# Optimization experiments

Measured on AMD Instinct MI355X. Metric: run time of the kernel, lower is better.

## Reference

```python
import jax, jax.numpy as jnp
import numpy as np

N = 50000   # nodes
E = 800000  # edges
F = 128     # n_features
H = 128     # n_hidden
LN_EPS = 1e-5


def setup_inputs() -> dict:
    key = jax.random.key(0)
    ks = jax.random.split(key, 11)
    s = 0.05
    return {
        "x": jax.random.normal(ks[0], (N, F), jnp.float32),
        "edge_index": jax.random.randint(ks[1], (2, E), 0, N, dtype=jnp.int64),
        "edge_attr": jax.random.uniform(ks[2], (E, 1), jnp.float32),
        "ln_gamma": jax.random.normal(ks[3], (F,), jnp.float32),
        "ln_beta": jax.random.normal(ks[4], (F,), jnp.float32),
        "W1": jax.random.normal(ks[5], (F, H), jnp.float32) * s,
        "b1": jax.random.normal(ks[6], (H,), jnp.float32) * s,
        "W2": jax.random.normal(ks[7], (H, H), jnp.float32) * s,
        "b2": jax.random.normal(ks[8], (H,), jnp.float32) * s,
        "W3": jax.random.normal(ks[9], (H, 1), jnp.float32) * s,
        "b3": jax.random.normal(ks[10], (1,), jnp.float32) * s,
    }


def _gcn_conv(x, W, b, row, col, ew, n_nodes):
    """PyG GCNConv: add self loops (weight 1), symmetric normalization,
    gather-scale-scatter aggregation, linear (no bias) + bias."""
    loop = jnp.arange(n_nodes, dtype=row.dtype)
    row_f = jnp.concatenate([row, loop])          # [E+N] source
    col_f = jnp.concatenate([col, loop])          # [E+N] target
    ew_f = jnp.concatenate([ew, jnp.ones((n_nodes,), ew.dtype)])
    deg = jax.ops.segment_sum(ew_f, col_f, num_segments=n_nodes)  # [N]
    dis = jnp.where(deg > 0, jax.lax.rsqrt(jnp.where(deg > 0, deg, 1.0)), 0.0)
    norm = dis[row_f] * ew_f * dis[col_f]          # [E+N]
    h = x @ W                                      # [N, out]
    msg = h[row_f] * norm[:, None]                 # [E+N, out] gather+scale
    out = jax.ops.segment_sum(msg, col_f, num_segments=n_nodes)  # scatter-add
    return out + b


def reference(x, edge_index, edge_attr, ln_gamma, ln_beta, W1, b1, W2, b2, W3, b3):
    x = jnp.nan_to_num(x, nan=0.0, posinf=0.0, neginf=0.0)
    ew = jnp.nan_to_num(edge_attr[:, 0], nan=0.0, posinf=1.0, neginf=0.0)  # [E]
    row, col = edge_index[0], edge_index[1]
    # input LayerNorm
    mu = jnp.mean(x, axis=-1, keepdims=True)
    var = jnp.mean(jnp.square(x - mu), axis=-1, keepdims=True)
    x = (x - mu) * jax.lax.rsqrt(var + LN_EPS) * ln_gamma + ln_beta
    # hidden GCN layers (dropout = identity in eval mode)
    x = jax.nn.relu(_gcn_conv(x, W1, b1, row, col, ew, N))
    x = jax.nn.relu(_gcn_conv(x, W2, b2, row, col, ew, N))
    # output layer
    return _gcn_conv(x, W3, b3, row, col, ew, N)  # [N, 1]
```

## Files before the change

### kernel.cpp

```cpp
#include <hip/hip_runtime.h>
#include <hip/hip_fp16.h>
#include <math.h>

#define NNODES 50000
#define NEDGES 800000
#define NF 128
#define BK 128
constexpr float LN_EPS = 1e-5f;

typedef short v8s __attribute__((ext_vector_type(8)));
typedef unsigned short v8u __attribute__((ext_vector_type(8)));
typedef float v4f __attribute__((ext_vector_type(4)));

__device__ __forceinline__ float clean0(float v) {
    return (isnan(v) || isinf(v)) ? 0.0f : v;
}
__device__ __forceinline__ float cleanw(float v) {
    if (isnan(v)) return 0.0f;
    if (isinf(v)) return v > 0.0f ? 1.0f : 0.0f;
    return v;
}
__device__ __forceinline__ int clampN(int v) {
    return min(max(v, 0), NNODES - 1);
}
__device__ __forceinline__ int pad8(int v) { return (v + 7) & ~7; }

__device__ __forceinline__ unsigned short f2bf(float f) {
    unsigned int u = __float_as_uint(f);
    return (unsigned short)((u + 0x7FFFu + ((u >> 16) & 1u)) >> 16);
}
__device__ __forceinline__ float bf2f(unsigned short h) {
    return __uint_as_float(((unsigned int)h) << 16);
}
__device__ __forceinline__ void split_bf(float v, unsigned short& h, unsigned short& l) {
    h = f2bf(v);
    l = f2bf(v - bf2f(h));
}

__global__ void k_build_ln(const int* __restrict__ ei, const float* __restrict__ ea,
                           int* __restrict__ cnt4, int2* __restrict__ bucket,
                           const float* __restrict__ x, const float* __restrict__ gamma,
                           const float* __restrict__ beta, unsigned short* __restrict__ z,
                           int nbb) {
    if ((int)blockIdx.x < nbb) {
        int e = blockIdx.x * 256 + threadIdx.x;
        if (e >= NEDGES) return;
        int r = clampN(ei[e]);
        int c = clampN(ei[NEDGES + e]);
        float w = cleanw(ea[e]);
        int s = e & 3;
        int pos = atomicAdd(&cnt4[(c << 2) + s], 1);
        if (pos < 32) bucket[(c << 7) + (s << 5) + pos] = make_int2(r, __float_as_int(w));
    } else {
        int bid = blockIdx.x - nbb;
        int n = (bid * 256 + threadIdx.x) >> 6;
        int lane = threadIdx.x & 63;
        if (n >= NNODES) return;
        float2 v = ((const float2*)(x + (size_t)n * NF))[lane];
        v.x = clean0(v.x); v.y = clean0(v.y);
        float s = v.x + v.y;
        for (int o = 32; o > 0; o >>= 1) s += __shfl_xor(s, o);
        float mu = s * (1.0f / NF);
        float dx = v.x - mu, dy = v.y - mu;
        float q = dx * dx + dy * dy;
        for (int o = 32; o > 0; o >>= 1) q += __shfl_xor(q, o);
        float rstd = rsqrtf(q * (1.0f / NF) + LN_EPS);
        float2 g = ((const float2*)gamma)[lane];
        float2 b = ((const float2*)beta)[lane];
        float ox = dx * rstd * g.x + b.x;
        float oy = dy * rstd * g.y + b.y;
        ((__half2*)z)[(size_t)n * 64 + lane] = __float22half2_rn(make_float2(ox, oy));
    }
}

__global__ void k_prep(int2* __restrict__ bucket, const int* __restrict__ cnt4,
                       int* __restrict__ cntp, float* __restrict__ dis,
                       const float* __restrict__ W1, const float* __restrict__ W2,
                       unsigned short* __restrict__ Wh1T, unsigned short* __restrict__ Wl1T,
                       unsigned short* __restrict__ Wh2T, unsigned short* __restrict__ Wl2T,
                       int nbn) {
    if ((int)blockIdx.x < nbn) {
        int n = blockIdx.x * 256 + threadIdx.x;
        if (n >= NNODES) return;
        int4 c4 = ((const int4*)cnt4)[n];
        int cs[4] = { min(c4.x, 32), min(c4.y, 32), min(c4.z, 32), min(c4.w, 32) };
        int base = n << 7;
        float d = 1.0f;
        for (int i = 0; i < cs[0]; i++) d += __int_as_float(bucket[base + i].y);
        int total = cs[0];
        #pragma unroll
        for (int s = 1; s < 4; s++) {
            int src = base + (s << 5);
            for (int i = 0; i < cs[s]; i++) {
                int2 rec = bucket[src + i];
                d += __int_as_float(rec.y);
                bucket[base + total + i] = rec;
            }
            total += cs[s];
        }
        for (int p = total; p < pad8(total); p++) bucket[base + p] = make_int2(0, 0);
        dis[n] = rsqrtf(d);
        cntp[n] = pad8(total);
    } else {
        int idx = (blockIdx.x - nbn) * 256 + threadIdx.x;
        int m = idx >> 14;
        int n = (idx >> 7) & 127;
        int k = idx & 127;
        const float* W = m ? W2 : W1;
        unsigned short* Wh = m ? Wh2T : Wh1T;
        unsigned short* Wl = m ? Wl2T : Wl1T;
        unsigned short h, l;
        split_bf(W[k * 128 + n], h, l);
        Wh[n * 128 + k] = h;
        Wl[n * 128 + k] = l;
    }
}

__global__ __launch_bounds__(256) void k_gemm_mfma(
        const unsigned short* __restrict__ Ain,
        const unsigned short* __restrict__ BhT, const unsigned short* __restrict__ BlT,
        const float* __restrict__ dis, unsigned short* __restrict__ C) {
    int w = threadIdx.x >> 6;
    int lane = threadIdx.x & 63;
    int m = lane & 15;
    int q = lane >> 4;
    int rowbase = blockIdx.x * 64 + w * 16;
    int arow = min(rowbase + m, NNODES - 1);

    const v8u* ap = (const v8u*)(Ain + (size_t)arow * NF);
    v8s afh[4], afl[4];
    #pragma unroll
    for (int c = 0; c < 4; c++) {
        v8u a = ap[c * 4 + q];
        #pragma unroll
        for (int j = 0; j < 8; j++) {
            float f = __half2float(__ushort_as_half(a[j]));
            unsigned short hh, ll;
            split_bf(f, hh, ll);
            afh[c][j] = (short)hh;
            afl[c][j] = (short)ll;
        }
    }

    float ds[4];
    #pragma unroll
    for (int r = 0; r < 4; r++) ds[r] = dis[min(rowbase + q * 4 + r, NNODES - 1)];

    for (int nt = 0; nt < 8; nt++) {
        int n0 = nt * 16;
        const v8s* bhp = (const v8s*)(BhT + (size_t)(n0 + m) * NF);
        const v8s* blp = (const v8s*)(BlT + (size_t)(n0 + m) * NF);
        v4f acc = {0.f, 0.f, 0.f, 0.f};
        #pragma unroll
        for (int c = 0; c < 4; c++) {
            v8s bh = bhp[c * 4 + q];
            v8s bl = blp[c * 4 + q];
            acc = __builtin_amdgcn_mfma_f32_16x16x32_bf16(afh[c], bh, acc, 0, 0, 0);
            acc = __builtin_amdgcn_mfma_f32_16x16x32_bf16(afh[c], bl, acc, 0, 0, 0);
            acc = __builtin_amdgcn_mfma_f32_16x16x32_bf16(afl[c], bh, acc, 0, 0, 0);
        }
        #pragma unroll
        for (int r = 0; r < 4; r++) {
            int gr = rowbase + q * 4 + r;
            if (gr < NNODES)
                C[(size_t)gr * NF + n0 + m] = __half_as_ushort(__float2half(acc[r] * ds[r]));
        }
    }
}

template <bool LAST>
__global__ __launch_bounds__(256) void k_aggregate(
        const unsigned short* __restrict__ h, const float* __restrict__ dis,
        const int* __restrict__ cntp, const int2* __restrict__ bucket,
        const float* __restrict__ bias, unsigned short* __restrict__ y,
        const float* __restrict__ W3, float* __restrict__ h3) {
    int n0 = (blockIdx.x * blockDim.x + threadIdx.x) >> 6;
    if (n0 >= NNODES) return;
    int n = __builtin_amdgcn_readfirstlane(n0);
    int lane = threadIdx.x & 63;
    const __half2* hp = (const __half2*)h;
    float2 acc = __half22float2(hp[(size_t)n * 64 + lane]);
    int beg = n << 7;
    int end = beg + cntp[n];
    int p = beg;
    if (p < end) {
        int2 rec[8];
        #pragma unroll
        for (int j = 0; j < 8; j++) rec[j] = bucket[p + j];
        p += 8;
        while (p < end) {
            float2 v[8];
            #pragma unroll
            for (int j = 0; j < 8; j++) v[j] = __half22float2(hp[(size_t)rec[j].x * 64 + lane]);
            int2 rec2[8];
            #pragma unroll
            for (int j = 0; j < 8; j++) rec2[j] = bucket[p + j];
            #pragma unroll
            for (int j = 0; j < 8; j++) {
                float w = __int_as_float(rec[j].y);
                acc.x += v[j].x * w;
                acc.y += v[j].y * w;
            }
            #pragma unroll
            for (int j = 0; j < 8; j++) rec[j] = rec2[j];
            p += 8;
        }
        float2 v[8];
        #pragma unroll
        for (int j = 0; j < 8; j++) v[j] = __half22float2(hp[(size_t)rec[j].x * 64 + lane]);
        #pragma unroll
        for (int j = 0; j < 8; j++) {
            float w = __int_as_float(rec[j].y);
            acc.x += v[j].x * w;
            acc.y += v[j].y * w;
        }
    }
    float dn = dis[n];
    float2 b = ((const float2*)bias)[lane];
    float ox = fmaxf(acc.x * dn + b.x, 0.0f);
    float oy = fmaxf(acc.y * dn + b.y, 0.0f);
    if (LAST) {
        float2 w3 = ((const float2*)W3)[lane];
        float s = ox * w3.x + oy * w3.y;
        for (int o = 32; o > 0; o >>= 1) s += __shfl_xor(s, o);
        if (lane == 0) h3[n] = s * dn;
    } else {
        ((__half2*)y)[(size_t)n * 64 + lane] = __float22half2_rn(make_float2(ox, oy));
    }
}

__global__ void k_agg_scalar(const float* __restrict__ h3, const float* __restrict__ dis,
                             const int* __restrict__ cntp, const int2* __restrict__ bucket,
                             const float* __restrict__ b3, float* __restrict__ out) {
    int n = blockIdx.x * blockDim.x + threadIdx.x;
    if (n >= NNODES) return;
    float acc = h3[n];
    int beg = n << 7;
    int end = beg + cntp[n];
    for (int p = beg; p + 4 <= end; p += 4) {
        int2 e0 = bucket[p], e1 = bucket[p + 1], e2 = bucket[p + 2], e3 = bucket[p + 3];
        float v0 = h3[e0.x], v1 = h3[e1.x], v2 = h3[e2.x], v3 = h3[e3.x];
        acc += v0 * __int_as_float(e0.y) + v1 * __int_as_float(e1.y)
             + v2 * __int_as_float(e2.y) + v3 * __int_as_float(e3.y);
    }
    out[n] = acc * dis[n] + b3[0];
}

extern "C" void kernel_launch(void* const* d_in, const int* in_sizes, int n_in,
                              void* d_out, int out_size, void* d_ws, size_t ws_size,
                              hipStream_t stream) {
    const float* x  = (const float*)d_in[0];
    const int*   ei = (const int*)d_in[1];
    const float* ea = (const float*)d_in[2];
    const float* g  = (const float*)d_in[3];
    const float* be = (const float*)d_in[4];
    const float* W1 = (const float*)d_in[5];
    const float* b1 = (const float*)d_in[6];
    const float* W2 = (const float*)d_in[7];
    const float* b2 = (const float*)d_in[8];
    const float* W3 = (const float*)d_in[9];
    const float* b3 = (const float*)d_in[10];
    float* out = (float*)d_out;

    char* ws = (char*)d_ws;
    size_t off = 0;
    auto alloc = [&](size_t bytes) {
        void* p = ws + off;
        off += (bytes + 255) & ~((size_t)255);
        return p;
    };
    unsigned short* zbuf = (unsigned short*)alloc((size_t)NNODES * NF * 2);
    unsigned short* hbuf = (unsigned short*)alloc((size_t)NNODES * NF * 2);
    float* dis    = (float*)alloc((size_t)NNODES * 4);
    int*   cnt4   = (int*)  alloc((size_t)NNODES * 4 * 4);
    int*   cntp   = (int*)  alloc((size_t)NNODES * 4);
    int2*  bucket = (int2*) alloc((size_t)NNODES * BK * 8);
    float* h3     = (float*)alloc((size_t)NNODES * 4);
    unsigned short* Wh1T = (unsigned short*)alloc(128 * 128 * 2);
    unsigned short* Wl1T = (unsigned short*)alloc(128 * 128 * 2);
    unsigned short* Wh2T = (unsigned short*)alloc(128 * 128 * 2);
    unsigned short* Wl2T = (unsigned short*)alloc(128 * 128 * 2);
    (void)ws_size; (void)in_sizes; (void)n_in; (void)out_size;

    const int NB_N = (NNODES + 255) / 256;
    const int NB_E = (NEDGES + 255) / 256;
    const int NB_W = (NNODES * 64 + 255) / 256;
    const int NB_G = (NNODES + 63) / 64;

    hipMemsetAsync(cnt4, 0, (size_t)NNODES * 16, stream);
    k_build_ln<<<NB_E + NB_W, 256, 0, stream>>>(ei, ea, cnt4, bucket,
                                                x, g, be, zbuf, NB_E);
    k_prep<<<NB_N + 128, 256, 0, stream>>>(bucket, cnt4, cntp, dis,
                                           W1, W2, Wh1T, Wl1T, Wh2T, Wl2T, NB_N);

    k_gemm_mfma<<<NB_G, 256, 0, stream>>>(zbuf, Wh1T, Wl1T, dis, hbuf);
    k_aggregate<false><<<NB_W, 256, 0, stream>>>(hbuf, dis, cntp, bucket, b1, zbuf,
                                                 nullptr, nullptr);
    k_gemm_mfma<<<NB_G, 256, 0, stream>>>(zbuf, Wh2T, Wl2T, dis, hbuf);
    k_aggregate<true><<<NB_W, 256, 0, stream>>>(hbuf, dis, cntp, bucket, b2, nullptr,
                                                W3, h3);
    k_agg_scalar<<<NB_N, 256, 0, stream>>>(h3, dis, cntp, bucket, b3, out);
}
```

Baseline: 296.2 us.

## Fuse all GCN stages into one persistent cooperative kernel with grid syncs

```diff
diff --git a/kernel.cpp b/kernel.cpp
--- a/kernel.cpp
+++ b/kernel.cpp
@@ -1,11 +1,15 @@
 #include <hip/hip_runtime.h>
 #include <hip/hip_fp16.h>
+#include <hip/hip_cooperative_groups.h>
 #include <math.h>
+
+namespace cg = cooperative_groups;
 
 #define NNODES 50000
 #define NEDGES 800000
 #define NF 128
 #define BK 128
+#define NTHR 256
 constexpr float LN_EPS = 1e-5f;
 
 typedef short v8s __attribute__((ext_vector_type(8)));
@@ -37,26 +41,154 @@
     l = f2bf(v - bf2f(h));
 }
 
-__global__ void k_build_ln(const int* __restrict__ ei, const float* __restrict__ ea,
-                           int* __restrict__ cnt4, int2* __restrict__ bucket,
-                           const float* __restrict__ x, const float* __restrict__ gamma,
-                           const float* __restrict__ beta, unsigned short* __restrict__ z,
-                           int nbb) {
-    if ((int)blockIdx.x < nbb) {
-        int e = blockIdx.x * 256 + threadIdx.x;
-        if (e >= NEDGES) return;
-        int r = clampN(ei[e]);
-        int c = clampN(ei[NEDGES + e]);
-        float w = cleanw(ea[e]);
+struct Params {
+    const int* ei; const float* ea;
+    const float* x; const float* g; const float* be;
+    const float* W1; const float* b1;
+    const float* W2; const float* b2;
+    const float* W3; const float* b3;
+    float* out;
+    unsigned short* zbuf; unsigned short* hbuf;
+    float* dis; int* cnt4; int* cntp; int2* bucket; float* h3;
+    unsigned short* Wh1T; unsigned short* Wl1T;
+    unsigned short* Wh2T; unsigned short* Wl2T;
+};
+
+__device__ __forceinline__ void gemm_phase(
+        const unsigned short* __restrict__ Ain,
+        const unsigned short* __restrict__ BhT, const unsigned short* __restrict__ BlT,
+        const float* __restrict__ dis, unsigned short* __restrict__ C) {
+    int w = threadIdx.x >> 6;
+    int lane = threadIdx.x & 63;
+    int m = lane & 15;
+    int q = lane >> 4;
+    const int ntiles = (NNODES + 63) / 64;
+    for (int tile = blockIdx.x; tile < ntiles; tile += gridDim.x) {
+        int rowbase = tile * 64 + w * 16;
+        int arow = min(rowbase + m, NNODES - 1);
+
+        const v8u* ap = (const v8u*)(Ain + (size_t)arow * NF);
+        v8s afh[4], afl[4];
+        #pragma unroll
+        for (int c = 0; c < 4; c++) {
+            v8u a = ap[c * 4 + q];
+            #pragma unroll
+            for (int j = 0; j < 8; j++) {
+                float f = __half2float(__ushort_as_half(a[j]));
+                unsigned short hh, ll;
+                split_bf(f, hh, ll);
+                afh[c][j] = (short)hh;
+                afl[c][j] = (short)ll;
+            }
+        }
+        float ds[4];
+        #pragma unroll
+        for (int r = 0; r < 4; r++) ds[r] = dis[min(rowbase + q * 4 + r, NNODES - 1)];
+
+        for (int nt = 0; nt < 8; nt++) {
+            int n0 = nt * 16;
+            const v8s* bhp = (const v8s*)(BhT + (size_t)(n0 + m) * NF);
+            const v8s* blp = (const v8s*)(BlT + (size_t)(n0 + m) * NF);
+            v4f acc = {0.f, 0.f, 0.f, 0.f};
+            #pragma unroll
+            for (int c = 0; c < 4; c++) {
+                v8s bh = bhp[c * 4 + q];
+                v8s bl = blp[c * 4 + q];
+                acc = __builtin_amdgcn_mfma_f32_16x16x32_bf16(afh[c], bh, acc, 0, 0, 0);
+                acc = __builtin_amdgcn_mfma_f32_16x16x32_bf16(afh[c], bl, acc, 0, 0, 0);
+                acc = __builtin_amdgcn_mfma_f32_16x16x32_bf16(afl[c], bh, acc, 0, 0, 0);
+            }
+            #pragma unroll
+            for (int r = 0; r < 4; r++) {
+                int gr = rowbase + q * 4 + r;
+                if (gr < NNODES)
+                    C[(size_t)gr * NF + n0 + m] = __half_as_ushort(__float2half(acc[r] * ds[r]));
+            }
+        }
+    }
+}
+
+template <bool LAST>
+__device__ __forceinline__ void agg_phase(
+        const unsigned short* __restrict__ h, const float* __restrict__ dis,
+        const int* __restrict__ cntp, const int2* __restrict__ bucket,
+        const float* __restrict__ bias, unsigned short* __restrict__ y,
+        const float* __restrict__ W3, float* __restrict__ h3) {
+    int lane = threadIdx.x & 63;
+    int wave0 = (blockIdx.x * NTHR + threadIdx.x) >> 6;
+    int nwaves = gridDim.x << 2;
+    const __half2* hp = (const __half2*)h;
+    for (int nn = wave0; nn < NNODES; nn += nwaves) {
+        int n = __builtin_amdgcn_readfirstlane(nn);
+        float2 acc = __half22float2(hp[(size_t)n * 64 + lane]);
+        int beg = n << 7;
+        int end = beg + cntp[n];
+        int p = beg;
+        if (p < end) {
+            int2 rec[8];
+            #pragma unroll
+            for (int j = 0; j < 8; j++) rec[j] = bucket[p + j];
+            p += 8;
+            while (p < end) {
+                float2 v[8];
+                #pragma unroll
+                for (int j = 0; j < 8; j++) v[j] = __half22float2(hp[(size_t)rec[j].x * 64 + lane]);
+                int2 rec2[8];
+                #pragma unroll
+                for (int j = 0; j < 8; j++) rec2[j] = bucket[p + j];
+                #pragma unroll
+                for (int j = 0; j < 8; j++) {
+                    float w = __int_as_float(rec[j].y);
+                    acc.x += v[j].x * w;
+                    acc.y += v[j].y * w;
+                }
+                #pragma unroll
+                for (int j = 0; j < 8; j++) rec[j] = rec2[j];
+                p += 8;
+            }
+            float2 v[8];
+            #pragma unroll
+            for (int j = 0; j < 8; j++) v[j] = __half22float2(hp[(size_t)rec[j].x * 64 + lane]);
+            #pragma unroll
+            for (int j = 0; j < 8; j++) {
+                float w = __int_as_float(rec[j].y);
+                acc.x += v[j].x * w;
+                acc.y += v[j].y * w;
+            }
+        }
+        float dn = dis[n];
+        float2 b = ((const float2*)bias)[lane];
+        float ox = fmaxf(acc.x * dn + b.x, 0.0f);
+        float oy = fmaxf(acc.y * dn + b.y, 0.0f);
+        if (LAST) {
+            float2 w3 = ((const float2*)W3)[lane];
+            float s = ox * w3.x + oy * w3.y;
+            for (int o = 32; o > 0; o >>= 1) s += __shfl_xor(s, o);
+            if (lane == 0) h3[n] = s * dn;
+        } else {
+            ((__half2*)y)[(size_t)n * 64 + lane] = __float22half2_rn(make_float2(ox, oy));
+        }
+    }
+}
+
+__global__ __launch_bounds__(256, 4) void k_mega(Params P) {
+    cg::grid_group grid = cg::this_grid();
+    const int tid = blockIdx.x * NTHR + threadIdx.x;
+    const int nthreads = gridDim.x * NTHR;
+    const int lane = threadIdx.x & 63;
+    const int wave0 = tid >> 6;
+    const int nwaves = gridDim.x << 2;
+
+    for (int e = tid; e < NEDGES; e += nthreads) {
+        int r = clampN(P.ei[e]);
+        int c = clampN(P.ei[NEDGES + e]);
+        float w = cleanw(P.ea[e]);
         int s = e & 3;
-        int pos = atomicAdd(&cnt4[(c << 2) + s], 1);
-        if (pos < 32) bucket[(c << 7) + (s << 5) + pos] = make_int2(r, __float_as_int(w));
-    } else {
-        int bid = blockIdx.x - nbb;
-        int n = (bid * 256 + threadIdx.x) >> 6;
-        int lane = threadIdx.x & 63;
-        if (n >= NNODES) return;
-        float2 v = ((const float2*)(x + (size_t)n * NF))[lane];
+        int pos = atomicAdd(&P.cnt4[(c << 2) + s], 1);
+        if (pos < 32) P.bucket[(c << 7) + (s << 5) + pos] = make_int2(r, __float_as_int(w));
+    }
+    for (int n = wave0; n < NNODES; n += nwaves) {
+        float2 v = ((const float2*)(P.x + (size_t)n * NF))[lane];
         v.x = clean0(v.x); v.y = clean0(v.y);
         float s = v.x + v.y;
         for (int o = 32; o > 0; o >>= 1) s += __shfl_xor(s, o);
@@ -65,203 +197,75 @@
         float q = dx * dx + dy * dy;
         for (int o = 32; o > 0; o >>= 1) q += __shfl_xor(q, o);
         float rstd = rsqrtf(q * (1.0f / NF) + LN_EPS);
-        float2 g = ((const float2*)gamma)[lane];
-        float2 b = ((const float2*)beta)[lane];
+        float2 g = ((const float2*)P.g)[lane];
+        float2 b = ((const float2*)P.be)[lane];
         float ox = dx * rstd * g.x + b.x;
         float oy = dy * rstd * g.y + b.y;
-        ((__half2*)z)[(size_t)n * 64 + lane] = __float22half2_rn(make_float2(ox, oy));
-    }
-}
-
-__global__ void k_prep(int2* __restrict__ bucket, const int* __restrict__ cnt4,
-                       int* __restrict__ cntp, float* __restrict__ dis,
-                       const float* __restrict__ W1, const float* __restrict__ W2,
-                       unsigned short* __restrict__ Wh1T, unsigned short* __restrict__ Wl1T,
-                       unsigned short* __restrict__ Wh2T, unsigned short* __restrict__ Wl2T,
-                       int nbn) {
-    if ((int)blockIdx.x < nbn) {
-        int n = blockIdx.x * 256 + threadIdx.x;
-        if (n >= NNODES) return;
-        int4 c4 = ((const int4*)cnt4)[n];
+        ((__half2*)P.zbuf)[(size_t)n * 64 + lane] = __float22half2_rn(make_float2(ox, oy));
+    }
+    grid.sync();
+
+    for (int n = tid; n < NNODES; n += nthreads) {
+        int4 c4 = ((const int4*)P.cnt4)[n];
         int cs[4] = { min(c4.x, 32), min(c4.y, 32), min(c4.z, 32), min(c4.w, 32) };
         int base = n << 7;
         float d = 1.0f;
-        for (int i = 0; i < cs[0]; i++) d += __int_as_float(bucket[base + i].y);
+        for (int i = 0; i < cs[0]; i++) d += __int_as_float(P.bucket[base + i].y);
         int total = cs[0];
         #pragma unroll
         for (int s = 1; s < 4; s++) {
             int src = base + (s << 5);
             for (int i = 0; i < cs[s]; i++) {
-                int2 rec = bucket[src + i];
+                int2 rec = P.bucket[src + i];
                 d += __int_as_float(rec.y);
-                bucket[base + total + i] = rec;
+                P.bucket[base + total + i] = rec;
             }
             total += cs[s];
         }
-        for (int p = total; p < pad8(total); p++) bucket[base + p] = make_int2(0, 0);
-        dis[n] = rsqrtf(d);
-        cntp[n] = pad8(total);
-    } else {
-        int idx = (blockIdx.x - nbn) * 256 + threadIdx.x;
+        for (int p = total; p < pad8(total); p++) P.bucket[base + p] = make_int2(0, 0);
+        P.dis[n] = rsqrtf(d);
+        P.cntp[n] = pad8(total);
+    }
+    for (int idx = tid; idx < 32768; idx += nthreads) {
         int m = idx >> 14;
         int n = (idx >> 7) & 127;
         int k = idx & 127;
-        const float* W = m ? W2 : W1;
-        unsigned short* Wh = m ? Wh2T : Wh1T;
-        unsigned short* Wl = m ? Wl2T : Wl1T;
+        const float* W = m ? P.W2 : P.W1;
+        unsigned short* Wh = m ? P.Wh2T : P.Wh1T;
+        unsigned short* Wl = m ? P.Wl2T : P.Wl1T;
         unsigned short h, l;
         split_bf(W[k * 128 + n], h, l);
         Wh[n * 128 + k] = h;
         Wl[n * 128 + k] = l;
     }
-}
-
-__global__ __launch_bounds__(256) void k_gemm_mfma(
-        const unsigned short* __restrict__ Ain,
-        const unsigned short* __restrict__ BhT, const unsigned short* __restrict__ BlT,
-        const float* __restrict__ dis, unsigned short* __restrict__ C) {
-    int w = threadIdx.x >> 6;
-    int lane = threadIdx.x & 63;
-    int m = lane & 15;
-    int q = lane >> 4;
-    int rowbase = blockIdx.x * 64 + w * 16;
-    int arow = min(rowbase + m, NNODES - 1);
-
-    const v8u* ap = (const v8u*)(Ain + (size_t)arow * NF);
-    v8s afh[4], afl[4];
-    #pragma unroll
-    for (int c = 0; c < 4; c++) {
-        v8u a = ap[c * 4 + q];
-        #pragma unroll
-        for (int j = 0; j < 8; j++) {
-            float f = __half2float(__ushort_as_half(a[j]));
-            unsigned short hh, ll;
-            split_bf(f, hh, ll);
-            afh[c][j] = (short)hh;
-            afl[c][j] = (short)ll;
-        }
-    }
-
-    float ds[4];
-    #pragma unroll
-    for (int r = 0; r < 4; r++) ds[r] = dis[min(rowbase + q * 4 + r, NNODES - 1)];
-
-    for (int nt = 0; nt < 8; nt++) {
-        int n0 = nt * 16;
-        const v8s* bhp = (const v8s*)(BhT + (size_t)(n0 + m) * NF);
-        const v8s* blp = (const v8s*)(BlT + (size_t)(n0 + m) * NF);
-        v4f acc = {0.f, 0.f, 0.f, 0.f};
-        #pragma unroll
-        for (int c = 0; c < 4; c++) {
-            v8s bh = bhp[c * 4 + q];
-            v8s bl = blp[c * 4 + q];
-            acc = __builtin_amdgcn_mfma_f32_16x16x32_bf16(afh[c], bh, acc, 0, 0, 0);
-            acc = __builtin_amdgcn_mfma_f32_16x16x32_bf16(afh[c], bl, acc, 0, 0, 0);
-            acc = __builtin_amdgcn_mfma_f32_16x16x32_bf16(afl[c], bh, acc, 0, 0, 0);
-        }
-        #pragma unroll
-        for (int r = 0; r < 4; r++) {
-            int gr = rowbase + q * 4 + r;
-            if (gr < NNODES)
-                C[(size_t)gr * NF + n0 + m] = __half_as_ushort(__float2half(acc[r] * ds[r]));
-        }
-    }
-}
-
-template <bool LAST>
-__global__ __launch_bounds__(256) void k_aggregate(
-        const unsigned short* __restrict__ h, const float* __restrict__ dis,
-        const int* __restrict__ cntp, const int2* __restrict__ bucket,
-        const float* __restrict__ bias, unsigned short* __restrict__ y,
-        const float* __restrict__ W3, float* __restrict__ h3) {
-    int n0 = (blockIdx.x * blockDim.x + threadIdx.x) >> 6;
-    if (n0 >= NNODES) return;
-    int n = __builtin_amdgcn_readfirstlane(n0);
-    int lane = threadIdx.x & 63;
-    const __half2* hp = (const __half2*)h;
-    float2 acc = __half22float2(hp[(size_t)n * 64 + lane]);
-    int beg = n << 7;
-    int end = beg + cntp[n];
-    int p = beg;
-    if (p < end) {
-        int2 rec[8];
-        #pragma unroll
-        for (int j = 0; j < 8; j++) rec[j] = bucket[p + j];
-        p += 8;
-        while (p < end) {
-            float2 v[8];
-            #pragma unroll
-            for (int j = 0; j < 8; j++) v[j] = __half22float2(hp[(size_t)rec[j].x * 64 + lane]);
-            int2 rec2[8];
-            #pragma unroll
-            for (int j = 0; j < 8; j++) rec2[j] = bucket[p + j];
-            #pragma unroll
-            for (int j = 0; j < 8; j++) {
-                float w = __int_as_float(rec[j].y);
-                acc.x += v[j].x * w;
-                acc.y += v[j].y * w;
-            }
-            #pragma unroll
-            for (int j = 0; j < 8; j++) rec[j] = rec2[j];
-            p += 8;
-        }
-        float2 v[8];
-        #pragma unroll
-        for (int j = 0; j < 8; j++) v[j] = __half22float2(hp[(size_t)rec[j].x * 64 + lane]);
-        #pragma unroll
-        for (int j = 0; j < 8; j++) {
-            float w = __int_as_float(rec[j].y);
-            acc.x += v[j].x * w;
-            acc.y += v[j].y * w;
-        }
-    }
-    float dn = dis[n];
-    float2 b = ((const float2*)bias)[lane];
-    float ox = fmaxf(acc.x * dn + b.x, 0.0f);
-    float oy = fmaxf(acc.y * dn + b.y, 0.0f);
-    if (LAST) {
-        float2 w3 = ((const float2*)W3)[lane];
-        float s = ox * w3.x + oy * w3.y;
-        for (int o = 32; o > 0; o >>= 1) s += __shfl_xor(s, o);
-        if (lane == 0) h3[n] = s * dn;
-    } else {
-        ((__half2*)y)[(size_t)n * 64 + lane] = __float22half2_rn(make_float2(ox, oy));
-    }
-}
-
-__global__ void k_agg_scalar(const float* __restrict__ h3, const float* __restrict__ dis,
-                             const int* __restrict__ cntp, const int2* __restrict__ bucket,
-                             const float* __restrict__ b3, float* __restrict__ out) {
-    int n = blockIdx.x * blockDim.x + threadIdx.x;
-    if (n >= NNODES) return;
-    float acc = h3[n];
-    int beg = n << 7;
-    int end = beg + cntp[n];
-    for (int p = beg; p + 4 <= end; p += 4) {
-        int2 e0 = bucket[p], e1 = bucket[p + 1], e2 = bucket[p + 2], e3 = bucket[p + 3];
-        float v0 = h3[e0.x], v1 = h3[e1.x], v2 = h3[e2.x], v3 = h3[e3.x];
-        acc += v0 * __int_as_float(e0.y) + v1 * __int_as_float(e1.y)
-             + v2 * __int_as_float(e2.y) + v3 * __int_as_float(e3.y);
-    }
-    out[n] = acc * dis[n] + b3[0];
+    grid.sync();
+
+    gemm_phase(P.zbuf, P.Wh1T, P.Wl1T, P.dis, P.hbuf);
+    grid.sync();
+    agg_phase<false>(P.hbuf, P.dis, P.cntp, P.bucket, P.b1, P.zbuf, nullptr, nullptr);
+    grid.sync();
+    gemm_phase(P.zbuf, P.Wh2T, P.Wl2T, P.dis, P.hbuf);
+    grid.sync();
+    agg_phase<true>(P.hbuf, P.dis, P.cntp, P.bucket, P.b2, nullptr, P.W3, P.h3);
+    grid.sync();
+    for (int n = tid; n < NNODES; n += nthreads) {
+        float acc = P.h3[n];
+        int beg = n << 7;
+        int end = beg + P.cntp[n];
+        for (int p = beg; p + 4 <= end; p += 4) {
+            int2 e0 = P.bucket[p], e1 = P.bucket[p + 1];
+            int2 e2 = P.bucket[p + 2], e3 = P.bucket[p + 3];
+            float v0 = P.h3[e0.x], v1 = P.h3[e1.x], v2 = P.h3[e2.x], v3 = P.h3[e3.x];
+            acc += v0 * __int_as_float(e0.y) + v1 * __int_as_float(e1.y)
+                 + v2 * __int_as_float(e2.y) + v3 * __int_as_float(e3.y);
+        }
+        P.out[n] = acc * P.dis[n] + P.b3[0];
+    }
 }
 
 extern "C" void kernel_launch(void* const* d_in, const int* in_sizes, int n_in,
                               void* d_out, int out_size, void* d_ws, size_t ws_size,
                               hipStream_t stream) {
-    const float* x  = (const float*)d_in[0];
-    const int*   ei = (const int*)d_in[1];
-    const float* ea = (const float*)d_in[2];
-    const float* g  = (const float*)d_in[3];
-    const float* be = (const float*)d_in[4];
-    const float* W1 = (const float*)d_in[5];
-    const float* b1 = (const float*)d_in[6];
-    const float* W2 = (const float*)d_in[7];
-    const float* b2 = (const float*)d_in[8];
-    const float* W3 = (const float*)d_in[9];
-    const float* b3 = (const float*)d_in[10];
-    float* out = (float*)d_out;
-
     char* ws = (char*)d_ws;
     size_t off = 0;
     auto alloc = [&](size_t bytes) {
@@ -269,35 +273,34 @@
         off += (bytes + 255) & ~((size_t)255);
         return p;
     };
-    unsigned short* zbuf = (unsigned short*)alloc((size_t)NNODES * NF * 2);
-    unsigned short* hbuf = (unsigned short*)alloc((size_t)NNODES * NF * 2);
-    float* dis    = (float*)alloc((size_t)NNODES * 4);
-    int*   cnt4   = (int*)  alloc((size_t)NNODES * 4 * 4);
-    int*   cntp   = (int*)  alloc((size_t)NNODES * 4);
-    int2*  bucket = (int2*) alloc((size_t)NNODES * BK * 8);
-    float* h3     = (float*)alloc((size_t)NNODES * 4);
-    unsigned short* Wh1T = (unsigned short*)alloc(128 * 128 * 2);
-    unsigned short* Wl1T = (unsigned short*)alloc(128 * 128 * 2);
-    unsigned short* Wh2T = (unsigned short*)alloc(128 * 128 * 2);
-    unsigned short* Wl2T = (unsigned short*)alloc(128 * 128 * 2);
+    Params P;
+    P.ei = (const int*)d_in[1];
+    P.ea = (const float*)d_in[2];
+    P.x  = (const float*)d_in[0];
+    P.g  = (const float*)d_in[3];
+    P.be = (const float*)d_in[4];
+    P.W1 = (const float*)d_in[5];  P.b1 = (const float*)d_in[6];
+    P.W2 = (const float*)d_in[7];  P.b2 = (const float*)d_in[8];
+    P.W3 = (const float*)d_in[9];  P.b3 = (const float*)d_in[10];
+    P.out = (float*)d_out;
+    P.zbuf = (unsigned short*)alloc((size_t)NNODES * NF * 2);
+    P.hbuf = (unsigned short*)alloc((size_t)NNODES * NF * 2);
+    P.dis  = (float*)alloc((size_t)NNODES * 4);
+    P.cnt4 = (int*)  alloc((size_t)NNODES * 16);
+    P.cntp = (int*)  alloc((size_t)NNODES * 4);
+    P.bucket = (int2*)alloc((size_t)NNODES * BK * 8);
+    P.h3   = (float*)alloc((size_t)NNODES * 4);
+    P.Wh1T = (unsigned short*)alloc(128 * 128 * 2);
+    P.Wl1T = (unsigned short*)alloc(128 * 128 * 2);
+    P.Wh2T = (unsigned short*)alloc(128 * 128 * 2);
+    P.Wl2T = (unsigned short*)alloc(128 * 128 * 2);
     (void)ws_size; (void)in_sizes; (void)n_in; (void)out_size;
 
-    const int NB_N = (NNODES + 255) / 256;
-    const int NB_E = (NEDGES + 255) / 256;
-    const int NB_W = (NNODES * 64 + 255) / 256;
-    const int NB_G = (NNODES + 63) / 64;
-
-    hipMemsetAsync(cnt4, 0, (size_t)NNODES * 16, stream);
-    k_build_ln<<<NB_E + NB_W, 256, 0, stream>>>(ei, ea, cnt4, bucket,
-                                                x, g, be, zbuf, NB_E);
-    k_prep<<<NB_N + 128, 256, 0, stream>>>(bucket, cnt4, cntp, dis,
-                                           W1, W2, Wh1T, Wl1T, Wh2T, Wl2T, NB_N);
-
-    k_gemm_mfma<<<NB_G, 256, 0, stream>>>(zbuf, Wh1T, Wl1T, dis, hbuf);
-    k_aggregate<false><<<NB_W, 256, 0, stream>>>(hbuf, dis, cntp, bucket, b1, zbuf,
-                                                 nullptr, nullptr);
-    k_gemm_mfma<<<NB_G, 256, 0, stream>>>(zbuf, Wh2T, Wl2T, dis, hbuf);
-    k_aggregate<true><<<NB_W, 256, 0, stream>>>(hbuf, dis, cntp, bucket, b2, nullptr,
-                                                W3, h3);
-    k_agg_scalar<<<NB_N, 256, 0, stream>>>(h3, dis, cntp, bucket, b3, out);
-}
+    hipMemsetAsync(P.cnt4, 0, (size_t)NNODES * 16, stream);
+
+    int perCU = 4;
+    hipOccupancyMaxActiveBlocksPerMultiprocessor(&perCU, k_mega, NTHR, 0);
+    int grid = min(1024, perCU * 256);
+    void* args[] = { &P };
+    hipLaunchCooperativeKernel((void*)k_mega, dim3(grid), dim3(NTHR), args, 0, stream);
+}
```

After: 711.4 us. 2.4x slower.
